# Performance work log

Hardware: AMD Instinct MI355X
Metric: run time of the kernel (lower is better)

The kernel has to match this reference:

```python
import jax, jax.numpy as jnp
import numpy as np

WAYS, SHOTS = 5, 5
F_DIM, HID = 1024, 512          # num_node_feats, int(1024*0.5)
BATCH = 2048                    # num_tasks
N = WAYS * SHOTS + 1            # 26 samples per episode
BN_EPS = 1e-5


def setup_inputs() -> dict:
    key = jax.random.key(0)
    ks = jax.random.split(key, 12)
    d = {"node_feats": jax.random.normal(ks[0], (BATCH, N, F_DIM), jnp.float32)}
    # conv1 (1x1): F_DIM -> HID, bn1; conv2: HID -> HID, bn2; conv4: HID -> F_DIM
    d["w1"] = jax.random.normal(ks[1], (HID, F_DIM), jnp.float32) * (1.0 / np.sqrt(F_DIM))
    d["b1"] = jax.random.normal(ks[2], (HID,), jnp.float32) * 0.01
    d["g1"] = jnp.ones((HID,), jnp.float32)
    d["be1"] = jnp.zeros((HID,), jnp.float32)
    d["m1"] = jax.random.normal(ks[3], (HID,), jnp.float32) * 0.1
    d["v1"] = jax.random.uniform(ks[4], (HID,), jnp.float32, 0.5, 1.5)
    d["w2"] = jax.random.normal(ks[5], (HID, HID), jnp.float32) * (1.0 / np.sqrt(HID))
    d["b2"] = jax.random.normal(ks[6], (HID,), jnp.float32) * 0.01
    d["g2"] = jnp.ones((HID,), jnp.float32)
    d["be2"] = jnp.zeros((HID,), jnp.float32)
    d["m2"] = jax.random.normal(ks[7], (HID,), jnp.float32) * 0.1
    d["v2"] = jax.random.uniform(ks[8], (HID,), jnp.float32, 0.5, 1.5)
    d["w3"] = jax.random.normal(ks[9], (F_DIM, HID), jnp.float32) * (1.0 / np.sqrt(HID))
    d["b3"] = jax.random.normal(ks[10], (F_DIM,), jnp.float32) * 0.01
    return d


def _conv1x1(x, w, b):
    # x: [B, Cin, N], w: [Cout, Cin] -> [B, Cout, N]
    return jnp.einsum('bcn,oc->bon', x, w) + b[None, :, None]


def _bn(x, g, be, m, v):
    # inference BatchNorm1d over channel dim of [B, C, N]
    scale = g / jnp.sqrt(v + BN_EPS)
    return (x - m[None, :, None]) * scale[None, :, None] + be[None, :, None]


def _forward(node_feats, w1, b1, g1, be1, m1, v1, w2, b2, g2, be2, m2, v2, w3, b3):
    B, n, F = node_feats.shape  # n == WAYS*SHOTS+1
    # in-place per-class mean on the transpose view also mutates node_feats in torch:
    sup = node_feats[:, :WAYS * SHOTS].reshape(B, WAYS, SHOTS, F)
    sup = jnp.broadcast_to(sup.mean(axis=2, keepdims=True), sup.shape).reshape(B, WAYS * SHOTS, F)
    nf = jnp.concatenate([sup, node_feats[:, WAYS * SHOTS:]], axis=1)  # [B, N, F]

    x = nf.transpose(0, 2, 1)  # [B, F, N]
    x = jax.nn.leaky_relu(_bn(_conv1x1(x, w1, b1), g1, be1, m1, v1), 0.01)
    x = jax.nn.leaky_relu(_bn(_conv1x1(x, w2, b2), g2, be2, m2, v2), 0.01)
    att = jax.nn.sigmoid(_conv1x1(x, w3, b3))  # [B, F, N]

    # sim_cal: cosine sim of u_ij = a_i*a_j*x_i vs v_ij = a_i*a_j*x_j, fused into matmuls.
    a = att.transpose(0, 2, 1)       # [B, N, F]
    a2 = a * a                       # attention squared
    P = a2 * nf                      # dot(u,v)   = (P P^T)[i,j]
    Q = a2 * nf * nf                 # ||u_ij||^2 = (Q a2^T)[i,j]
    dots = jnp.einsum('bif,bjf->bij', P, P)    # [B, N, N]
    n2 = jnp.einsum('bif,bjf->bij', Q, a2)     # [B, N, N]
    nrm = jnp.sqrt(n2)
    sim = dots / (nrm * nrm.transpose(0, 2, 1))
    pred = jnp.stack([sim, 1.0 - sim], axis=1)  # [B, 2, N, N]
    return jnp.clip(pred, 0.0, 1.0)


def reference(node_feats, w1, b1, g1, be1, m1, v1, w2, b2, g2, be2, m2, v2, w3, b3):
    return _forward(node_feats, w1, b1, g1, be1, m1, v1, w2, b2, g2, be2, m2, v2, w3, b3)
```

## Files before the change

### kernel.cpp

```cpp
#include <hip/hip_runtime.h>
#include <hip/hip_bf16.h>
#include <math.h>

typedef __bf16 bf16_t;
typedef bf16_t bf16x8 __attribute__((ext_vector_type(8)));
typedef float f32x4 __attribute__((ext_vector_type(4)));

#define WAYS 5
#define SHOTS 5
#define F_DIM 1024
#define HID 512
#define BATCH 2048
#define NN 26
#define NC 6
#define MROWS (BATCH * NC)

#define S1 (HID * F_DIM)
#define S2 (HID * HID)
#define S3 (F_DIM * HID)

__global__ __launch_bounds__(256)
void cvt_all_kernel(const float* __restrict__ w1, const float* __restrict__ w2,
                    const float* __restrict__ w3, bf16_t* __restrict__ out) {
    int i = (blockIdx.x * 256 + threadIdx.x) * 4;
    if (i >= S1 + S2 + S3) return;
    const float* src;
    int j = i;
    if (i < S1)            { src = w1; }
    else if (i < S1 + S2)  { src = w2; j = i - S1; }
    else                   { src = w3; j = i - S1 - S2; }
    float4 v = *(const float4*)(src + j);
    out[i + 0] = (bf16_t)v.x;
    out[i + 1] = (bf16_t)v.y;
    out[i + 2] = (bf16_t)v.z;
    out[i + 3] = (bf16_t)v.w;
}

__global__ __launch_bounds__(128)
void nfc_kernel(const float* __restrict__ node, bf16_t* __restrict__ nfc_b) {
    int row = blockIdx.x;
    int b = row / NC;
    int w = row - b * NC;
    int f = threadIdx.x * 8;
    const float* src = node + (size_t)b * NN * F_DIM;
    float acc[8];
    if (w < WAYS) {
        #pragma unroll
        for (int e = 0; e < 8; ++e) acc[e] = 0.f;
        #pragma unroll
        for (int s = 0; s < SHOTS; ++s) {
            const float* r = src + (size_t)(w * SHOTS + s) * F_DIM + f;
            float4 v0 = *(const float4*)r;
            float4 v1 = *(const float4*)(r + 4);
            acc[0] += v0.x; acc[1] += v0.y; acc[2] += v0.z; acc[3] += v0.w;
            acc[4] += v1.x; acc[5] += v1.y; acc[6] += v1.z; acc[7] += v1.w;
        }
        #pragma unroll
        for (int e = 0; e < 8; ++e) acc[e] *= 0.2f;
    } else {
        const float* r = src + (size_t)25 * F_DIM + f;
        float4 v0 = *(const float4*)r;
        float4 v1 = *(const float4*)(r + 4);
        acc[0] = v0.x; acc[1] = v0.y; acc[2] = v0.z; acc[3] = v0.w;
        acc[4] = v1.x; acc[5] = v1.y; acc[6] = v1.z; acc[7] = v1.w;
    }
    bf16x8 ob;
    #pragma unroll
    for (int e = 0; e < 8; ++e) ob[e] = (bf16_t)acc[e];
    *(bf16x8*)(nfc_b + (size_t)row * F_DIM + f) = ob;
}

template<int EPI, int TN>
__global__ __launch_bounds__(256)
void gemm_bt(const bf16_t* __restrict__ A, const bf16_t* __restrict__ W,
             bf16_t* __restrict__ C, int M, int N, int K,
             const float* __restrict__ bias, const float* __restrict__ gam,
             const float* __restrict__ bet, const float* __restrict__ mu,
             const float* __restrict__ var) {
    constexpr int NI = TN / 32;
    __shared__ bf16_t As[128 * 32];
    __shared__ bf16_t Bs[TN * 32];
    const int tid = threadIdx.x;
    const int lane = tid & 63, wid = tid >> 6;
    const int bm = blockIdx.y * 128, bn = blockIdx.x * TN;
    const int l15 = lane & 15, quad = lane >> 4;
    const int wm = (wid & 1) * 64, wn = (wid >> 1) * (TN / 2);

    const int srowA = wid * 32;
    const int srowB = wid * (TN / 4);
    const int lrow = lane >> 2;
    const int lcol = (lane & 3) * 8;
    const bf16_t* gA = A + (size_t)(bm + srowA + lrow) * K + lcol;
    const bf16_t* gB = W + (size_t)(bn + srowB + lrow) * K + lcol;
    bf16_t* lA = &As[srowA * 32];
    bf16_t* lB = &Bs[srowB * 32];

    f32x4 acc[4][NI] = {};

    for (int k0 = 0; k0 < K; k0 += 32) {
        __syncthreads();
        #pragma unroll
        for (int q = 0; q < 2; ++q)
            __builtin_amdgcn_global_load_lds(
                (const __attribute__((address_space(1))) void*)(gA + (size_t)q * 16 * K + k0),
                (__attribute__((address_space(3))) void*)(lA + q * 16 * 32), 16, 0, 0);
        #pragma unroll
        for (int q = 0; q < TN / 64; ++q)
            __builtin_amdgcn_global_load_lds(
                (const __attribute__((address_space(1))) void*)(gB + (size_t)q * 16 * K + k0),
                (__attribute__((address_space(3))) void*)(lB + q * 16 * 32), 16, 0, 0);
        __syncthreads();
        bf16x8 af[4], bfr[NI];
        #pragma unroll
        for (int mi = 0; mi < 4; ++mi)
            af[mi] = *(const bf16x8*)&As[(wm + mi * 16 + l15) * 32 + quad * 8];
        #pragma unroll
        for (int ni = 0; ni < NI; ++ni)
            bfr[ni] = *(const bf16x8*)&Bs[(wn + ni * 16 + l15) * 32 + quad * 8];
        #pragma unroll
        for (int mi = 0; mi < 4; ++mi)
            #pragma unroll
            for (int ni = 0; ni < NI; ++ni)
                acc[mi][ni] = __builtin_amdgcn_mfma_f32_16x16x32_bf16(af[mi], bfr[ni], acc[mi][ni], 0, 0, 0);
    }

    #pragma unroll
    for (int ni = 0; ni < NI; ++ni) {
        const int n = bn + wn + ni * 16 + l15;
        float s, t;
        if constexpr (EPI == 0) {
            float sg = gam[n] * rsqrtf(var[n] + 1e-5f);
            s = sg;
            t = (bias[n] - mu[n]) * sg + bet[n];
        } else {
            s = 1.0f;
            t = bias[n];
        }
        #pragma unroll
        for (int mi = 0; mi < 4; ++mi) {
            const int m = bm + wm + mi * 16 + quad * 4;
            #pragma unroll
            for (int r = 0; r < 4; ++r) {
                float y = acc[mi][ni][r] * s + t;
                if constexpr (EPI == 0) {
                    y = y > 0.0f ? y : 0.01f * y;
                } else {
                    y = 1.0f / (1.0f + __expf(-y));
                }
                C[(size_t)(m + r) * N + n] = (bf16_t)y;
            }
        }
    }
}

__global__ __launch_bounds__(256)
void sim_kernel(const bf16_t* __restrict__ nfc, const bf16_t* __restrict__ att,
                float* __restrict__ out) {
    __shared__ float sx[NC * F_DIM];
    __shared__ float sa[NC * F_DIM];
    __shared__ float dmat[NC * NC], n2mat[NC * NC], simc[NC * NC];
    const int b = blockIdx.x, tid = threadIdx.x;
    const bf16_t* xs = nfc + (size_t)b * NC * F_DIM;
    const bf16_t* as = att + (size_t)b * NC * F_DIM;
    for (int i = tid * 8; i < NC * F_DIM; i += 256 * 8) {
        bf16x8 vx = *(const bf16x8*)&xs[i];
        bf16x8 va = *(const bf16x8*)&as[i];
        #pragma unroll
        for (int e = 0; e < 8; ++e) { sx[i + e] = (float)vx[e]; sa[i + e] = (float)va[e]; }
    }
    __syncthreads();
    const int lane = tid & 63, wid = tid >> 6;
    const int ti[21] = {0,0,0,0,0,0,1,1,1,1,1,2,2,2,2,3,3,3,4,4,5};
    const int tj[21] = {0,1,2,3,4,5,1,2,3,4,5,2,3,4,5,3,4,5,4,5,5};
    for (int t = wid; t < 21; t += 4) {
        const int i = ti[t], j = tj[t];
        float d = 0.f, qij = 0.f, qji = 0.f;
        for (int f = lane; f < F_DIM; f += 64) {
            float ai = sa[i * F_DIM + f], aj = sa[j * F_DIM + f];
            float xi = sx[i * F_DIM + f], xj = sx[j * F_DIM + f];
            float a2i = ai * ai, a2j = aj * aj;
            float pi = a2i * xi, pj = a2j * xj;
            d   += pi * pj;
            qij += pi * xi * a2j;
            qji += pj * xj * a2i;
        }
        #pragma unroll
        for (int off = 32; off > 0; off >>= 1) {
            d   += __shfl_xor(d, off);
            qij += __shfl_xor(qij, off);
            qji += __shfl_xor(qji, off);
        }
        if (lane == 0) {
            dmat[i * NC + j] = d; dmat[j * NC + i] = d;
            n2mat[i * NC + j] = qij; n2mat[j * NC + i] = qji;
        }
    }
    __syncthreads();
    if (tid < NC * NC) {
        int i = tid / NC, j = tid - (tid / NC) * NC;
        simc[tid] = dmat[tid] / sqrtf(n2mat[i * NC + j] * n2mat[j * NC + i]);
    }
    __syncthreads();
    float* o = out + (size_t)b * (2 * NN * NN);
    for (int e = tid; e < 2 * NN * NN; e += 256) {
        int ch = e / (NN * NN);
        int rem = e - ch * (NN * NN);
        int i = rem / NN, j = rem - (rem / NN) * NN;
        float s = simc[(i / 5) * NC + (j / 5)];
        float v = ch ? 1.0f - s : s;
        v = fminf(fmaxf(v, 0.0f), 1.0f);
        o[e] = v;
    }
}

extern "C" void kernel_launch(void* const* d_in, const int* in_sizes, int n_in,
                              void* d_out, int out_size, void* d_ws, size_t ws_size,
                              hipStream_t stream) {
    const float* node = (const float*)d_in[0];
    const float* w1  = (const float*)d_in[1];
    const float* b1  = (const float*)d_in[2];
    const float* g1  = (const float*)d_in[3];
    const float* be1 = (const float*)d_in[4];
    const float* m1  = (const float*)d_in[5];
    const float* v1  = (const float*)d_in[6];
    const float* w2  = (const float*)d_in[7];
    const float* b2  = (const float*)d_in[8];
    const float* g2  = (const float*)d_in[9];
    const float* be2 = (const float*)d_in[10];
    const float* m2  = (const float*)d_in[11];
    const float* v2  = (const float*)d_in[12];
    const float* w3  = (const float*)d_in[13];
    const float* b3  = (const float*)d_in[14];
    float* out = (float*)d_out;

    char* ws = (char*)d_ws;
    size_t off = 0;
    bf16_t* wall  = (bf16_t*)(ws + off); off += (size_t)(S1 + S2 + S3) * 2;
    bf16_t* w1b = wall, *w2b = wall + S1, *w3b = wall + S1 + S2;
    bf16_t* nfc_b = (bf16_t*)(ws + off); off += (size_t)MROWS * F_DIM * 2;
    bf16_t* x1    = (bf16_t*)(ws + off); off += (size_t)MROWS * HID * 2;
    bf16_t* x2    = (bf16_t*)(ws + off); off += (size_t)MROWS * HID * 2;
    bf16_t* attb  = (bf16_t*)(ws + off); off += (size_t)MROWS * F_DIM * 2;

    cvt_all_kernel<<<((S1 + S2 + S3) / 4 + 255) / 256, 256, 0, stream>>>(w1, w2, w3, wall);
    nfc_kernel<<<MROWS, 128, 0, stream>>>(node, nfc_b);
    gemm_bt<0, 64><<<dim3(HID / 64, MROWS / 128), 256, 0, stream>>>(
        nfc_b, w1b, x1, MROWS, HID, F_DIM, b1, g1, be1, m1, v1);
    gemm_bt<0, 64><<<dim3(HID / 64, MROWS / 128), 256, 0, stream>>>(
        x1, w2b, x2, MROWS, HID, HID, b2, g2, be2, m2, v2);
    gemm_bt<1, 128><<<dim3(F_DIM / 128, MROWS / 128), 256, 0, stream>>>(
        x2, w3b, attb, MROWS, F_DIM, HID, b3, nullptr, nullptr, nullptr, nullptr);
    sim_kernel<<<BATCH, 256, 0, stream>>>(nfc_b, attb, out);
}
```

Before: 445.5 us.

## Fuse three MLP GEMMs into one kernel keeping intermediates in LDS

Replaces the three separate tiled GEMM launches with a single fused kernel that processes 48-row tiles through all three 1x1 conv layers. The hidden activations stay in padded shared memory instead of round-tripping through global memory. Operands are loaded straight from global into registers with software double-buffering rather than staged through LDS. The cost is that each block re-reads the full weight matrices and the grid is only 256 blocks. LDS use per block is also large, which limits occupancy.

```diff
diff --git a/kernel.cpp b/kernel.cpp
--- a/kernel.cpp
+++ b/kernel.cpp
@@ -18,6 +18,9 @@
 #define S1 (HID * F_DIM)
 #define S2 (HID * HID)
 #define S3 (F_DIM * HID)
+
+#define TM 48
+#define PADX 520
 
 __global__ __launch_bounds__(256)
 void cvt_all_kernel(const float* __restrict__ w1, const float* __restrict__ w2,
@@ -70,84 +73,158 @@
     *(bf16x8*)(nfc_b + (size_t)row * F_DIM + f) = ob;
 }
 
-template<int EPI, int TN>
 __global__ __launch_bounds__(256)
-void gemm_bt(const bf16_t* __restrict__ A, const bf16_t* __restrict__ W,
-             bf16_t* __restrict__ C, int M, int N, int K,
-             const float* __restrict__ bias, const float* __restrict__ gam,
-             const float* __restrict__ bet, const float* __restrict__ mu,
-             const float* __restrict__ var) {
-    constexpr int NI = TN / 32;
-    __shared__ bf16_t As[128 * 32];
-    __shared__ bf16_t Bs[TN * 32];
+void fused_mlp(const bf16_t* __restrict__ nfc, const bf16_t* __restrict__ w1b,
+               const bf16_t* __restrict__ w2b, const bf16_t* __restrict__ w3b,
+               bf16_t* __restrict__ att,
+               const float* __restrict__ b1, const float* __restrict__ g1,
+               const float* __restrict__ be1, const float* __restrict__ m1,
+               const float* __restrict__ v1,
+               const float* __restrict__ b2, const float* __restrict__ g2,
+               const float* __restrict__ be2, const float* __restrict__ m2,
+               const float* __restrict__ v2,
+               const float* __restrict__ b3) {
+    __shared__ bf16_t X1[TM * PADX];
+    __shared__ bf16_t X2[TM * PADX];
     const int tid = threadIdx.x;
-    const int lane = tid & 63, wid = tid >> 6;
-    const int bm = blockIdx.y * 128, bn = blockIdx.x * TN;
+    const int lane = tid & 63;
+    const int wv = tid >> 6;
     const int l15 = lane & 15, quad = lane >> 4;
-    const int wm = (wid & 1) * 64, wn = (wid >> 1) * (TN / 2);
-
-    const int srowA = wid * 32;
-    const int srowB = wid * (TN / 4);
-    const int lrow = lane >> 2;
-    const int lcol = (lane & 3) * 8;
-    const bf16_t* gA = A + (size_t)(bm + srowA + lrow) * K + lcol;
-    const bf16_t* gB = W + (size_t)(bn + srowB + lrow) * K + lcol;
-    bf16_t* lA = &As[srowA * 32];
-    bf16_t* lB = &Bs[srowB * 32];
-
-    f32x4 acc[4][NI] = {};
-
-    for (int k0 = 0; k0 < K; k0 += 32) {
-        __syncthreads();
-        #pragma unroll
-        for (int q = 0; q < 2; ++q)
-            __builtin_amdgcn_global_load_lds(
-                (const __attribute__((address_space(1))) void*)(gA + (size_t)q * 16 * K + k0),
-                (__attribute__((address_space(3))) void*)(lA + q * 16 * 32), 16, 0, 0);
-        #pragma unroll
-        for (int q = 0; q < TN / 64; ++q)
-            __builtin_amdgcn_global_load_lds(
-                (const __attribute__((address_space(1))) void*)(gB + (size_t)q * 16 * K + k0),
-                (__attribute__((address_space(3))) void*)(lB + q * 16 * 32), 16, 0, 0);
-        __syncthreads();
-        bf16x8 af[4], bfr[NI];
-        #pragma unroll
-        for (int mi = 0; mi < 4; ++mi)
-            af[mi] = *(const bf16x8*)&As[(wm + mi * 16 + l15) * 32 + quad * 8];
-        #pragma unroll
-        for (int ni = 0; ni < NI; ++ni)
-            bfr[ni] = *(const bf16x8*)&Bs[(wn + ni * 16 + l15) * 32 + quad * 8];
-        #pragma unroll
-        for (int mi = 0; mi < 4; ++mi)
-            #pragma unroll
-            for (int ni = 0; ni < NI; ++ni)
-                acc[mi][ni] = __builtin_amdgcn_mfma_f32_16x16x32_bf16(af[mi], bfr[ni], acc[mi][ni], 0, 0, 0);
-    }
-
-    #pragma unroll
-    for (int ni = 0; ni < NI; ++ni) {
-        const int n = bn + wn + ni * 16 + l15;
-        float s, t;
-        if constexpr (EPI == 0) {
-            float sg = gam[n] * rsqrtf(var[n] + 1e-5f);
-            s = sg;
-            t = (bias[n] - mu[n]) * sg + bet[n];
-        } else {
-            s = 1.0f;
-            t = bias[n];
-        }
-        #pragma unroll
-        for (int mi = 0; mi < 4; ++mi) {
-            const int m = bm + wm + mi * 16 + quad * 4;
+    const int bm = blockIdx.x * TM;
+    const int nb = wv * 128;
+
+    f32x4 acc[3][8];
+
+    auto mmac = [&](bf16x8 (&af)[6], bf16x8 (&bf)[16]) {
+        #pragma unroll
+        for (int kk = 0; kk < 2; ++kk)
+            #pragma unroll
+            for (int mt = 0; mt < 3; ++mt)
+                #pragma unroll
+                for (int nt = 0; nt < 8; ++nt)
+                    acc[mt][nt] = __builtin_amdgcn_mfma_f32_16x16x32_bf16(
+                        af[mt * 2 + kk], bf[nt * 2 + kk], acc[mt][nt], 0, 0, 0);
+    };
+    auto ldB = [&](bf16x8 (&bf)[16], const bf16_t* W, int K, int c) {
+        #pragma unroll
+        for (int nt = 0; nt < 8; ++nt)
+            #pragma unroll
+            for (int kk = 0; kk < 2; ++kk)
+                bf[nt * 2 + kk] = *(const bf16x8*)(W + (size_t)(nb + nt * 16 + l15) * K
+                                                   + c * 64 + kk * 32 + quad * 8);
+    };
+    auto ldA1 = [&](bf16x8 (&af)[6], int c) {
+        #pragma unroll
+        for (int mt = 0; mt < 3; ++mt)
+            #pragma unroll
+            for (int kk = 0; kk < 2; ++kk)
+                af[mt * 2 + kk] = *(const bf16x8*)(nfc + (size_t)(bm + mt * 16 + l15) * F_DIM
+                                                    + c * 64 + kk * 32 + quad * 8);
+    };
+    auto ldAx = [&](bf16x8 (&af)[6], int which, int c) {
+        #pragma unroll
+        for (int mt = 0; mt < 3; ++mt)
+            #pragma unroll
+            for (int kk = 0; kk < 2; ++kk) {
+                int idx = (mt * 16 + l15) * PADX + c * 64 + kk * 32 + quad * 8;
+                af[mt * 2 + kk] = which ? *(const bf16x8*)&X2[idx] : *(const bf16x8*)&X1[idx];
+            }
+    };
+
+    bf16x8 aF0[6], aF1[6], bF0[16], bF1[16];
+
+    #pragma unroll
+    for (int mt = 0; mt < 3; ++mt)
+        #pragma unroll
+        for (int nt = 0; nt < 8; ++nt)
+            acc[mt][nt] = (f32x4){0.f, 0.f, 0.f, 0.f};
+    ldA1(aF0, 0); ldB(bF0, w1b, F_DIM, 0);
+    for (int c = 0; c < 16; c += 2) {
+        ldA1(aF1, c + 1); ldB(bF1, w1b, F_DIM, c + 1);
+        mmac(aF0, bF0);
+        if (c + 2 < 16) { ldA1(aF0, c + 2); ldB(bF0, w1b, F_DIM, c + 2); }
+        mmac(aF1, bF1);
+    }
+    #pragma unroll
+    for (int nt = 0; nt < 8; ++nt) {
+        const int n = nb + nt * 16 + l15;
+        const float sg = g1[n] * rsqrtf(v1[n] + 1e-5f);
+        const float tt = (b1[n] - m1[n]) * sg + be1[n];
+        #pragma unroll
+        for (int mt = 0; mt < 3; ++mt) {
+            const int row = mt * 16 + quad * 4;
             #pragma unroll
             for (int r = 0; r < 4; ++r) {
-                float y = acc[mi][ni][r] * s + t;
-                if constexpr (EPI == 0) {
-                    y = y > 0.0f ? y : 0.01f * y;
-                } else {
+                float y = acc[mt][nt][r] * sg + tt;
+                y = y > 0.f ? y : 0.01f * y;
+                X1[(row + r) * PADX + n] = (bf16_t)y;
+            }
+        }
+    }
+    __syncthreads();
+
+    #pragma unroll
+    for (int mt = 0; mt < 3; ++mt)
+        #pragma unroll
+        for (int nt = 0; nt < 8; ++nt)
+            acc[mt][nt] = (f32x4){0.f, 0.f, 0.f, 0.f};
+    ldB(bF0, w2b, HID, 0);
+    for (int c = 0; c < 8; c += 2) {
+        ldB(bF1, w2b, HID, c + 1);
+        ldAx(aF0, 0, c);
+        mmac(aF0, bF0);
+        if (c + 2 < 8) ldB(bF0, w2b, HID, c + 2);
+        ldAx(aF1, 0, c + 1);
+        mmac(aF1, bF1);
+    }
+    #pragma unroll
+    for (int nt = 0; nt < 8; ++nt) {
+        const int n = nb + nt * 16 + l15;
+        const float sg = g2[n] * rsqrtf(v2[n] + 1e-5f);
+        const float tt = (b2[n] - m2[n]) * sg + be2[n];
+        #pragma unroll
+        for (int mt = 0; mt < 3; ++mt) {
+            const int row = mt * 16 + quad * 4;
+            #pragma unroll
+            for (int r = 0; r < 4; ++r) {
+                float y = acc[mt][nt][r] * sg + tt;
+                y = y > 0.f ? y : 0.01f * y;
+                X2[(row + r) * PADX + n] = (bf16_t)y;
+            }
+        }
+    }
+    __syncthreads();
+
+    #pragma unroll
+    for (int h = 0; h < 2; ++h) {
+        const bf16_t* w3h = w3b + (size_t)(h * 512) * HID;
+        #pragma unroll
+        for (int mt = 0; mt < 3; ++mt)
+            #pragma unroll
+            for (int nt = 0; nt < 8; ++nt)
+                acc[mt][nt] = (f32x4){0.f, 0.f, 0.f, 0.f};
+        ldB(bF0, w3h, HID, 0);
+        for (int c = 0; c < 8; c += 2) {
+            ldB(bF1, w3h, HID, c + 1);
+            ldAx(aF0, 1, c);
+            mmac(aF0, bF0);
+            if (c + 2 < 8) ldB(bF0, w3h, HID, c + 2);
+            ldAx(aF1, 1, c + 1);
+            mmac(aF1, bF1);
+        }
+        #pragma unroll
+        for (int nt = 0; nt < 8; ++nt) {
+            const int n = h * 512 + nb + nt * 16 + l15;
+            const float tt = b3[n];
+            #pragma unroll
+            for (int mt = 0; mt < 3; ++mt) {
+                const int m = bm + mt * 16 + quad * 4;
+                #pragma unroll
+                for (int r = 0; r < 4; ++r) {
+                    float y = acc[mt][nt][r] + tt;
                     y = 1.0f / (1.0f + __expf(-y));
+                    att[(size_t)(m + r) * F_DIM + n] = (bf16_t)y;
                 }
-                C[(size_t)(m + r) * N + n] = (bf16_t)y;
             }
         }
     }
@@ -238,17 +315,12 @@
     bf16_t* wall  = (bf16_t*)(ws + off); off += (size_t)(S1 + S2 + S3) * 2;
     bf16_t* w1b = wall, *w2b = wall + S1, *w3b = wall + S1 + S2;
     bf16_t* nfc_b = (bf16_t*)(ws + off); off += (size_t)MROWS * F_DIM * 2;
-    bf16_t* x1    = (bf16_t*)(ws + off); off += (size_t)MROWS * HID * 2;
-    bf16_t* x2    = (bf16_t*)(ws + off); off += (size_t)MROWS * HID * 2;
     bf16_t* attb  = (bf16_t*)(ws + off); off += (size_t)MROWS * F_DIM * 2;
 
     cvt_all_kernel<<<((S1 + S2 + S3) / 4 + 255) / 256, 256, 0, stream>>>(w1, w2, w3, wall);
     nfc_kernel<<<MROWS, 128, 0, stream>>>(node, nfc_b);
-    gemm_bt<0, 64><<<dim3(HID / 64, MROWS / 128), 256, 0, stream>>>(
-        nfc_b, w1b, x1, MROWS, HID, F_DIM, b1, g1, be1, m1, v1);
-    gemm_bt<0, 64><<<dim3(HID / 64, MROWS / 128), 256, 0, stream>>>(
-        x1, w2b, x2, MROWS, HID, HID, b2, g2, be2, m2, v2);
-    gemm_bt<1, 128><<<dim3(F_DIM / 128, MROWS / 128), 256, 0, stream>>>(
-        x2, w3b, attb, MROWS, F_DIM, HID, b3, nullptr, nullptr, nullptr, nullptr);
+    fused_mlp<<<MROWS / TM, 256, 0, stream>>>(nfc_b, w1b, w2b, w3b, attb,
+                                              b1, g1, be1, m1, v1,
+                                              b2, g2, be2, m2, v2, b3);
     sim_kernel<<<BATCH, 256, 0, stream>>>(nfc_b, attb, out);
 }
```

Measured after the change: 468.4 us. +5.2%, slower.
